# Optimization experiments

Measured on AMD Instinct MI355X. Metric: run time of the kernel, lower is better.

The kernel has to match this reference:

```python
import jax, jax.numpy as jnp
import numpy as np

DIM = 1024
EXP = 4
B, S = 4, 4096


def setup_inputs() -> dict:
    key = jax.random.key(0)
    ks = jax.random.split(key, 20)
    d, h = DIM, DIM * EXP
    sc = 1.0 / np.sqrt(d)
    inp = {
        "x": jax.random.normal(ks[0], (B, S, d), dtype=jnp.float32),
        # attention linears, stored [in, out] so y = x @ W + b
        "wq": jax.random.normal(ks[1], (d, d), jnp.float32) * sc,
        "bq": jnp.zeros((d,), jnp.float32),
        "wk": jax.random.normal(ks[2], (d, d), jnp.float32) * sc,
        "bk": jnp.zeros((d,), jnp.float32),
        "wv": jax.random.normal(ks[3], (d, d), jnp.float32) * sc,
        "bv": jnp.zeros((d,), jnp.float32),
        "wo": jax.random.normal(ks[4], (d, d), jnp.float32) * sc,
        "bo": jnp.zeros((d,), jnp.float32),
        # FFN
        "w1": jax.random.normal(ks[5], (d, h), jnp.float32) * sc,
        "b1": jnp.zeros((h,), jnp.float32),
        "w2": jax.random.normal(ks[6], (h, d), jnp.float32) * (1.0 / np.sqrt(h)),
        "b2": jnp.zeros((d,), jnp.float32),
        # LayerNorms
        "g1": jnp.ones((d,), jnp.float32),
        "beta1": jnp.zeros((d,), jnp.float32),
        "g2": jnp.ones((d,), jnp.float32),
        "beta2": jnp.zeros((d,), jnp.float32),
    }
    return inp


def _layernorm(x, g, b, eps=1e-5):
    mu = jnp.mean(x, axis=-1, keepdims=True)
    var = jnp.mean(jnp.square(x - mu), axis=-1, keepdims=True)
    return (x - mu) * jax.lax.rsqrt(var + eps) * g + b


def _block(x, wq, bq, wk, bk, wv, bv, wo, bo, w1, b1, w2, b2, g1, beta1, g2, beta2):
    d = x.shape[-1]
    # attention sub-block (single head, full [B,S,S] scores as in source)
    h = _layernorm(x, g1, beta1)
    q = h @ wq + bq
    k = h @ wk + bk
    v = h @ wv + bv
    scores = jnp.einsum("bsd,btd->bst", q, k) / jnp.sqrt(jnp.asarray(d, x.dtype))
    attn = jax.nn.softmax(scores, axis=-1)
    a = jnp.einsum("bst,btd->bsd", attn, v) @ wo + bo
    x = x + a
    # FFN sub-block (exact GELU, matching torch nn.GELU default)
    h2 = _layernorm(x, g2, beta2)
    f = jax.nn.gelu(h2 @ w1 + b1, approximate=False) @ w2 + b2
    return x + f


def reference(x, wq, bq, wk, bk, wv, bv, wo, bo, w1, b1, w2, b2, g1, beta1, g2, beta2):
    return _block(x, wq, bq, wk, bk, wv, bv, wo, bo, w1, b1, w2, b2, g1, beta1, g2, beta2)
```

## Files before the change

kernel.cpp:

```cpp
#include <hip/hip_runtime.h>
#include <hip/hip_bf16.h>
#include <cstdint>

typedef __bf16 bf16;
typedef __bf16 bf16x8 __attribute__((ext_vector_type(8)));
typedef __bf16 bf16x4 __attribute__((ext_vector_type(4)));
typedef float f32x4 __attribute__((ext_vector_type(4)));

#define DEV __device__ __forceinline__

DEV float wred_sum(float v) {
#pragma unroll
  for (int off = 32; off > 0; off >>= 1) v += __shfl_xor(v, off, 64);
  return v;
}
DEV float wred_max(float v) {
#pragma unroll
  for (int off = 32; off > 0; off >>= 1) v = fmaxf(v, __shfl_xor(v, off, 64));
  return v;
}

__global__ void convT_kernel(const float* __restrict__ in, bf16* __restrict__ out,
                             int K, int N) {
  __shared__ float t[32][33];
  const int n0 = blockIdx.x * 32, k0 = blockIdx.y * 32;
  const int tx = threadIdx.x & 31, ty = threadIdx.x >> 5;
#pragma unroll
  for (int i = 0; i < 4; i++)
    t[ty + 8 * i][tx] = in[(long)(k0 + ty + 8 * i) * N + n0 + tx];
  __syncthreads();
#pragma unroll
  for (int i = 0; i < 4; i++)
    out[(long)(n0 + ty + 8 * i) * K + k0 + tx] = (bf16)t[tx][ty + 8 * i];
}

__global__ void transpose_bf16(const bf16* __restrict__ in, bf16* __restrict__ out,
                               int ldin, int ldout) {
  __shared__ bf16 t[32][33];
  const int c0 = blockIdx.x * 32, r0 = blockIdx.y * 32;
  const int tx = threadIdx.x & 31, ty = threadIdx.x >> 5;
#pragma unroll
  for (int i = 0; i < 4; i++)
    t[ty + 8 * i][tx] = in[(long)(r0 + ty + 8 * i) * ldin + c0 + tx];
  __syncthreads();
#pragma unroll
  for (int i = 0; i < 4; i++)
    out[(long)(c0 + ty + 8 * i) * ldout + r0 + tx] = t[tx][ty + 8 * i];
}

__global__ void ln_bf16_kernel(const float* __restrict__ x, const float* __restrict__ g,
                               const float* __restrict__ be, bf16* __restrict__ out) {
  const long row = blockIdx.x;
  const int tid = threadIdx.x;
  const float4 v = ((const float4*)(x + row * 1024))[tid];
  float s = v.x + v.y + v.z + v.w;
  float s2 = v.x * v.x + v.y * v.y + v.z * v.z + v.w * v.w;
  __shared__ float rs_[4], rs2_[4];
  s = wred_sum(s);
  s2 = wred_sum(s2);
  const int wave = tid >> 6, lane = tid & 63;
  if (lane == 0) { rs_[wave] = s; rs2_[wave] = s2; }
  __syncthreads();
  s = rs_[0] + rs_[1] + rs_[2] + rs_[3];
  s2 = rs2_[0] + rs2_[1] + rs2_[2] + rs2_[3];
  const float mu = s * (1.0f / 1024.0f);
  const float var = s2 * (1.0f / 1024.0f) - mu * mu;
  const float rstd = rsqrtf(var + 1e-5f);
  const float4 gg = ((const float4*)g)[tid];
  const float4 bb = ((const float4*)be)[tid];
  bf16x4 o;
  o[0] = (bf16)((v.x - mu) * rstd * gg.x + bb.x);
  o[1] = (bf16)((v.y - mu) * rstd * gg.y + bb.y);
  o[2] = (bf16)((v.z - mu) * rstd * gg.z + bb.z);
  o[3] = (bf16)((v.w - mu) * rstd * gg.w + bb.w);
  *(bf16x4*)(out + row * 1024 + tid * 4) = o;
}

__global__ void softmax_kernel(bf16* __restrict__ p) {
  const long row = blockIdx.x;
  bf16* pr = p + row * 4096;
  const int tid = threadIdx.x;
  bf16x8 a = *(const bf16x8*)(pr + tid * 16);
  bf16x8 b = *(const bf16x8*)(pr + tid * 16 + 8);
  float v[16];
#pragma unroll
  for (int i = 0; i < 8; i++) { v[i] = (float)a[i]; v[8 + i] = (float)b[i]; }
  float mx = -1e30f;
#pragma unroll
  for (int i = 0; i < 16; i++) mx = fmaxf(mx, v[i]);
  __shared__ float red1[4], red2[4];
  mx = wred_max(mx);
  const int wave = tid >> 6, lane = tid & 63;
  if (lane == 0) red1[wave] = mx;
  __syncthreads();
  mx = fmaxf(fmaxf(red1[0], red1[1]), fmaxf(red1[2], red1[3]));
  float s = 0.0f;
#pragma unroll
  for (int i = 0; i < 16; i++) { v[i] = __expf(v[i] - mx); s += v[i]; }
  s = wred_sum(s);
  if (lane == 0) red2[wave] = s;
  __syncthreads();
  s = red2[0] + red2[1] + red2[2] + red2[3];
  const float inv = 1.0f / s;
#pragma unroll
  for (int i = 0; i < 8; i++) { a[i] = (bf16)(v[i] * inv); b[i] = (bf16)(v[8 + i] * inv); }
  *(bf16x8*)(pr + tid * 16) = a;
  *(bf16x8*)(pr + tid * 16 + 8) = b;
}

enum { EPI_BF16 = 0, EPI_QKV = 1, EPI_GELU = 2, EPI_F32RES = 3 };

DEV void stage16(const bf16* g, bf16* l) {
  __builtin_amdgcn_global_load_lds((const __attribute__((address_space(1))) void*)g,
                                   (__attribute__((address_space(3))) void*)l, 16, 0, 0);
}

template <int EPI>
__global__ __launch_bounds__(256)
void gemm128(const bf16* __restrict__ A, const bf16* __restrict__ B,
             const float* __restrict__ bias, const float* __restrict__ resid,
             void* Cout, int M, int N, int K,
             int lda, int ldb, int ldc, float alpha) {
  extern __shared__ __align__(16) char smem[];
  bf16* sA = (bf16*)smem;
  bf16* sB = sA + 3 * 8192;
  int flat = (int)(blockIdx.y * gridDim.x + blockIdx.x);
  {
    const int nwg = (int)(gridDim.x * gridDim.y);
    const int qq = nwg >> 3, rr = nwg & 7;
    const int xcd = flat & 7, idx = flat >> 3;
    flat = (xcd < rr ? xcd * (qq + 1) : rr * (qq + 1) + (xcd - rr) * qq) + idx;
  }
  const int bix = flat % (int)gridDim.x, biy = flat / (int)gridDim.x;
  const int tid = threadIdx.x;
  const int lane = tid & 63;
  const int wid = tid >> 6;
  const int q = lane >> 4, r16 = lane & 15;
  const int wr = wid >> 1, wc = wid & 1;
  const long m0 = (long)biy * 128;
  const long n0 = (long)bix * 128;
  const int srow = tid >> 3;
  const int gcol = ((tid & 7) ^ (srow & 7)) * 8;
  const long lda32 = (long)lda * 32, ldb32 = (long)ldb * 32;
  const bf16* Ag = A + (m0 + srow) * (long)lda + gcol;
  const bf16* Bg = B + (n0 + srow) * (long)ldb + gcol;
  const int NT = K >> 6;
  const int swz = r16 * 64 + ((q ^ (r16 & 7)) * 8);
  const int abase = wr * 4096 + swz;
  const int bbase = wc * 4096 + swz;
  f32x4 acc[4][4] = {};

#pragma unroll
  for (int blk = 0; blk < 4; ++blk) {
    stage16(Ag + blk * lda32, sA + tid * 8 + blk * 2048);
    stage16(Bg + blk * ldb32, sB + tid * 8 + blk * 2048);
  }
  if (NT > 1) {
#pragma unroll
    for (int blk = 0; blk < 4; ++blk) {
      stage16(Ag + 64 + blk * lda32, sA + 8192 + tid * 8 + blk * 2048);
      stage16(Bg + 64 + blk * ldb32, sB + 8192 + tid * 8 + blk * 2048);
    }
    asm volatile("s_waitcnt vmcnt(8)" ::: "memory");
  } else {
    asm volatile("s_waitcnt vmcnt(0)" ::: "memory");
  }
  __builtin_amdgcn_sched_barrier(0);
  __builtin_amdgcn_s_barrier();
  __builtin_amdgcn_sched_barrier(0);

  int bx = 0, bs = 16384;
  for (int t = 0; t < NT; ++t) {
    if (t + 2 < NT) {
      const bf16* Agn = Ag + (t + 2) * 64;
      const bf16* Bgn = Bg + (t + 2) * 64;
#pragma unroll
      for (int blk = 0; blk < 4; ++blk) {
        stage16(Agn + blk * lda32, sA + bs + tid * 8 + blk * 2048);
        stage16(Bgn + blk * ldb32, sB + bs + tid * 8 + blk * 2048);
      }
    }
    const bf16* sAb = sA + bx;
    const bf16* sBb = sB + bx;
    bf16x8 a0[4], a1[4], b0[4], b1[4];
#pragma unroll
    for (int i = 0; i < 4; ++i) {
      a0[i] = *(const bf16x8*)(sAb + (abase + i * 1024));
      a1[i] = *(const bf16x8*)(sAb + ((abase + i * 1024) ^ 32));
      b0[i] = *(const bf16x8*)(sBb + (bbase + i * 1024));
      b1[i] = *(const bf16x8*)(sBb + ((bbase + i * 1024) ^ 32));
    }
#pragma unroll
    for (int i = 0; i < 4; ++i)
#pragma unroll
      for (int j = 0; j < 4; ++j) {
        acc[i][j] = __builtin_amdgcn_mfma_f32_16x16x32_bf16(b0[j], a0[i], acc[i][j], 0, 0, 0);
        acc[i][j] = __builtin_amdgcn_mfma_f32_16x16x32_bf16(b1[j], a1[i], acc[i][j], 0, 0, 0);
      }
    if (t + 2 < NT) {
      asm volatile("s_waitcnt vmcnt(8)" ::: "memory");
    } else if (t + 1 < NT) {
      asm volatile("s_waitcnt vmcnt(0)" ::: "memory");
    }
    if (t + 1 < NT) {
      __builtin_amdgcn_sched_barrier(0);
      __builtin_amdgcn_s_barrier();
      __builtin_amdgcn_sched_barrier(0);
    }
    bx += 8192; if (bx == 24576) bx = 0;
    bs += 8192; if (bs == 24576) bs = 0;
  }

#pragma unroll
  for (int i = 0; i < 4; ++i) {
    const long row = m0 + wr * 64 + i * 16 + r16;
#pragma unroll
    for (int j = 0; j < 4; ++j) {
      const int ncol = (int)n0 + wc * 64 + j * 16 + q * 4;
      float4 b4 = make_float4(0.f, 0.f, 0.f, 0.f);
      if (bias != nullptr) b4 = *(const float4*)(bias + ncol);
      float v0 = acc[i][j][0] * alpha + b4.x;
      float v1 = acc[i][j][1] * alpha + b4.y;
      float v2 = acc[i][j][2] * alpha + b4.z;
      float v3 = acc[i][j][3] * alpha + b4.w;
      if (EPI == EPI_F32RES) {
        const long idx = row * (long)ldc + ncol;
        const float4 rr = *(const float4*)(resid + idx);
        const float4 o = make_float4(v0 + rr.x, v1 + rr.y, v2 + rr.z, v3 + rr.w);
        *(float4*)((float*)Cout + idx) = o;
      } else {
        bf16x4 o;
        o[0] = (bf16)v0; o[1] = (bf16)v1; o[2] = (bf16)v2; o[3] = (bf16)v3;
        *(bf16x4*)((bf16*)Cout + row * (long)ldc + ncol) = o;
      }
    }
  }
}

template <int EPI>
__global__ __launch_bounds__(512, 2)
void gemm256(const bf16* __restrict__ A, const bf16* __restrict__ B,
             const float* __restrict__ bias, const float* bias2, const float* bias3,
             const float* resid, void* Cout, int M, int N, int K,
             int lda, int ldb, int ldc, float alpha) {
  extern __shared__ __align__(16) char smem[];
  bf16* sA = (bf16*)smem;
  bf16* sB = sA + 32768;
  const int tid = threadIdx.x;
  const int lane = tid & 63;
  const int wid = tid >> 6;
  const int q = lane >> 4, r16 = lane & 15;
  const int wr = wid >> 2, wc = wid & 3;
  const long m0 = (long)blockIdx.y * 256;
  const long n0 = (long)blockIdx.x * 256;
  const int srow = tid >> 3;
  const int gcol = ((tid & 7) ^ (srow & 7)) * 8;
  const long lda64 = (long)lda * 64, ldb64 = (long)ldb * 64;
  const bf16* AgT = A + (m0 + srow) * (long)lda + gcol;
  const bf16* BgT = B + (n0 + srow) * (long)ldb + gcol;
  bf16* lA = sA + tid * 8;
  bf16* lB = sB + tid * 8;
  const int NT = K >> 6;
  const int swz = r16 * 64 + ((q ^ (r16 & 7)) * 8);
  const int abase = wr * 8192 + swz;
  const int bbase = (wc >> 1) * 8192 + (wc & 1) * 4096 + swz;

  f32x4 acc[8][4] = {};

  stage16(BgT,             lB);
  stage16(BgT + ldb64,     lB + 4096);
  stage16(BgT + 2 * ldb64, lB + 8192);
  stage16(BgT + 3 * ldb64, lB + 12288);
  stage16(AgT,             lA);
  stage16(AgT + lda64,     lA + 4096);
  stage16(AgT + 2 * lda64, lA + 8192);
  stage16(AgT + 3 * lda64, lA + 12288);
  if (NT > 1) {
    stage16(BgT + 64,             lB + 16384);
    stage16(BgT + 64 + ldb64,     lB + 16384 + 4096);
    stage16(BgT + 64 + 2 * ldb64, lB + 16384 + 8192);
    stage16(BgT + 64 + 3 * ldb64, lB + 16384 + 12288);
    asm volatile("s_waitcnt vmcnt(4)" ::: "memory");
  } else {
    asm volatile("s_waitcnt vmcnt(0)" ::: "memory");
  }
  __builtin_amdgcn_sched_barrier(0);
  __builtin_amdgcn_s_barrier();
  __builtin_amdgcn_sched_barrier(0);

  for (int t = 0; t < NT; ++t) {
    const int bx = (t & 1) * 16384;
    const int nbx = 16384 - bx;
    const bf16* sAb = sA + bx;
    const bf16* sBb = sB + bx;
    bf16x8 b0[4], b1[4];
#pragma unroll
    for (int p = 0; p < 4; ++p) {
      if (p == 0) {
#pragma unroll
        for (int n = 0; n < 4; ++n) {
          b0[n] = *(const bf16x8*)(sBb + (bbase + n * 1024));
          b1[n] = *(const bf16x8*)(sBb + ((bbase + n * 1024) ^ 32));
        }
      }
      const int ab = abase + p * 2048;
      const bf16x8 a00 = *(const bf16x8*)(sAb + ab);
      const bf16x8 a10 = *(const bf16x8*)(sAb + (ab ^ 32));
      const bf16x8 a01 = *(const bf16x8*)(sAb + (ab + 1024));
      const bf16x8 a11 = *(const bf16x8*)(sAb + ((ab + 1024) ^ 32));
      if (p == 0 && t + 1 < NT) {
        stage16(AgT + 64,         lA + nbx);
        stage16(AgT + 64 + lda64, lA + nbx + 4096);
      }
      if (p == 1 && t + 1 < NT) {
        stage16(AgT + 64 + 2 * lda64, lA + nbx + 8192);
        stage16(AgT + 64 + 3 * lda64, lA + nbx + 12288);
      }
      if (p == 2 && t + 2 < NT) {
        stage16(BgT + 128,         lB + bx);
        stage16(BgT + 128 + ldb64, lB + bx + 4096);
      }
      if (p == 3 && t + 2 < NT) {
        stage16(BgT + 128 + 2 * ldb64, lB + bx + 8192);
        stage16(BgT + 128 + 3 * ldb64, lB + bx + 12288);
      }
      __builtin_amdgcn_sched_barrier(0);
      __builtin_amdgcn_s_barrier();
      __builtin_amdgcn_sched_barrier(0);
      __builtin_amdgcn_s_setprio(1);
#pragma unroll
      for (int n = 0; n < 4; ++n) {
        acc[2 * p][n]     = __builtin_amdgcn_mfma_f32_16x16x32_bf16(b0[n], a00, acc[2 * p][n], 0, 0, 0);
        acc[2 * p][n]     = __builtin_amdgcn_mfma_f32_16x16x32_bf16(b1[n], a10, acc[2 * p][n], 0, 0, 0);
        acc[2 * p + 1][n] = __builtin_amdgcn_mfma_f32_16x16x32_bf16(b0[n], a01, acc[2 * p + 1][n], 0, 0, 0);
        acc[2 * p + 1][n] = __builtin_amdgcn_mfma_f32_16x16x32_bf16(b1[n], a11, acc[2 * p + 1][n], 0, 0, 0);
      }
      __builtin_amdgcn_s_setprio(0);
      if (p == 3) {
        if (t + 2 < NT)      asm volatile("s_waitcnt vmcnt(4)" ::: "memory");
        else if (t + 1 < NT) asm volatile("s_waitcnt vmcnt(0)" ::: "memory");
      }
      __builtin_amdgcn_sched_barrier(0);
      __builtin_amdgcn_s_barrier();
      __builtin_amdgcn_sched_barrier(0);
    }
    AgT += 64;
    BgT += 64;
  }

#pragma unroll
  for (int m = 0; m < 8; ++m) {
    const long row = m0 + wr * 128 + m * 16 + r16;
#pragma unroll
    for (int n = 0; n < 4; ++n) {
      const int ncol = (int)n0 + wc * 64 + n * 16 + q * 4;
      float4 b4 = make_float4(0.f, 0.f, 0.f, 0.f);
      if (EPI == EPI_QKV) {
        const int band = ncol >> 10;
        const float* bsel = band == 0 ? bias : (band == 1 ? bias2 : bias3);
        b4 = *(const float4*)(bsel + (ncol & 1023));
      } else if (bias != nullptr) {
        b4 = *(const float4*)(bias + ncol);
      }
      float v0 = acc[m][n][0] * alpha + b4.x;
      float v1 = acc[m][n][1] * alpha + b4.y;
      float v2 = acc[m][n][2] * alpha + b4.z;
      float v3 = acc[m][n][3] * alpha + b4.w;
      if (EPI == EPI_GELU) {
        v0 = 0.5f * v0 * (1.0f + erff(v0 * 0.70710678118654752f));
        v1 = 0.5f * v1 * (1.0f + erff(v1 * 0.70710678118654752f));
        v2 = 0.5f * v2 * (1.0f + erff(v2 * 0.70710678118654752f));
        v3 = 0.5f * v3 * (1.0f + erff(v3 * 0.70710678118654752f));
      }
      if (EPI == EPI_F32RES) {
        const long idx = row * (long)ldc + ncol;
        const float4 rr = *(const float4*)(resid + idx);
        const float4 o = make_float4(v0 + rr.x, v1 + rr.y, v2 + rr.z, v3 + rr.w);
        *(float4*)((float*)Cout + idx) = o;
      } else {
        bf16x4 o;
        o[0] = (bf16)v0; o[1] = (bf16)v1; o[2] = (bf16)v2; o[3] = (bf16)v3;
        *(bf16x4*)((bf16*)Cout + row * (long)ldc + ncol) = o;
      }
    }
  }
}

extern "C" void kernel_launch(void* const* d_in, const int* in_sizes, int n_in,
                              void* d_out, int out_size, void* d_ws, size_t ws_size,
                              hipStream_t stream) {
  const float* x  = (const float*)d_in[0];
  const float* wq = (const float*)d_in[1];
  const float* bq = (const float*)d_in[2];
  const float* wk = (const float*)d_in[3];
  const float* bk = (const float*)d_in[4];
  const float* wv = (const float*)d_in[5];
  const float* bv = (const float*)d_in[6];
  const float* wo = (const float*)d_in[7];
  const float* bo = (const float*)d_in[8];
  const float* w1 = (const float*)d_in[9];
  const float* b1 = (const float*)d_in[10];
  const float* w2 = (const float*)d_in[11];
  const float* b2 = (const float*)d_in[12];
  const float* g1 = (const float*)d_in[13];
  const float* be1 = (const float*)d_in[14];
  const float* g2 = (const float*)d_in[15];
  const float* be2 = (const float*)d_in[16];

  static int attr_done = 0;
  if (!attr_done) {
    attr_done = 1;
    hipFuncSetAttribute(reinterpret_cast<const void*>(&gemm256<EPI_QKV>),
                        hipFuncAttributeMaxDynamicSharedMemorySize, 131072);
    hipFuncSetAttribute(reinterpret_cast<const void*>(&gemm256<EPI_BF16>),
                        hipFuncAttributeMaxDynamicSharedMemorySize, 131072);
    hipFuncSetAttribute(reinterpret_cast<const void*>(&gemm256<EPI_GELU>),
                        hipFuncAttributeMaxDynamicSharedMemorySize, 131072);
    hipFuncSetAttribute(reinterpret_cast<const void*>(&gemm256<EPI_F32RES>),
                        hipFuncAttributeMaxDynamicSharedMemorySize, 131072);
    hipFuncSetAttribute(reinterpret_cast<const void*>(&gemm128<EPI_BF16>),
                        hipFuncAttributeMaxDynamicSharedMemorySize, 98304);
    hipFuncSetAttribute(reinterpret_cast<const void*>(&gemm128<EPI_F32RES>),
                        hipFuncAttributeMaxDynamicSharedMemorySize, 98304);
  }

  const long MB = 1 << 20;
  char* ws = (char*)d_ws;
  char* ob = (char*)d_out;
  bf16* WQKV = (bf16*)(ws + 0 * MB);
  bf16* WO   = (bf16*)(ws + 6 * MB);
  bf16* W1   = (bf16*)(ws + 8 * MB);
  bf16* W2   = (bf16*)(ws + 16 * MB);
  bf16* H    = (bf16*)(ws + 24 * MB);
  bf16* P    = (bf16*)(ob + 0 * MB);
  bf16* QKVb = (bf16*)(ob + 32 * MB);
  bf16* Vt   = (bf16*)(ob + 56 * MB);
  float* OUT = (float*)d_out;
  const dim3 blk(256);
  const dim3 blk512(512);
  const size_t SMEM = 131072;
  const size_t SMEM128 = 98304;

  convT_kernel<<<dim3(32, 32), blk, 0, stream>>>(wq, WQKV, 1024, 1024);
  convT_kernel<<<dim3(32, 32), blk, 0, stream>>>(wk, WQKV + 1024 * 1024, 1024, 1024);
  convT_kernel<<<dim3(32, 32), blk, 0, stream>>>(wv, WQKV + 2048 * 1024, 1024, 1024);
  convT_kernel<<<dim3(32, 32), blk, 0, stream>>>(wo, WO, 1024, 1024);
  convT_kernel<<<dim3(128, 32), blk, 0, stream>>>(w1, W1, 1024, 4096);
  convT_kernel<<<dim3(32, 128), blk, 0, stream>>>(w2, W2, 4096, 1024);
  ln_bf16_kernel<<<16384, blk, 0, stream>>>(x, g1, be1, H);
  for (int z = 0; z < 4; z++) {
    const long zo = (long)z * 4096 * 1024;
    gemm256<EPI_QKV><<<dim3(12, 16), blk512, SMEM, stream>>>(
        H + zo, WQKV, bq, bk, bv, nullptr, QKVb,
        4096, 3072, 1024, 1024, 1024, 3072, 1.0f);
    transpose_bf16<<<dim3(32, 128), blk, 0, stream>>>(QKVb + 2048, Vt, 3072, 4096);
    gemm256<EPI_BF16><<<dim3(16, 16), blk512, SMEM, stream>>>(
        QKVb, QKVb + 1024, nullptr, nullptr, nullptr, nullptr, P,
        4096, 4096, 1024, 3072, 3072, 4096, 1.0f / 32.0f);
    softmax_kernel<<<4096, blk, 0, stream>>>(P);
    gemm128<EPI_BF16><<<dim3(8, 32), blk, SMEM128, stream>>>(
        P, Vt, nullptr, nullptr, H + zo,
        4096, 1024, 4096, 4096, 4096, 1024, 1.0f);
  }
  gemm256<EPI_F32RES><<<dim3(4, 64), blk512, SMEM, stream>>>(
      H, WO, bo, nullptr, nullptr, x, OUT,
      16384, 1024, 1024, 1024, 1024, 1024, 1.0f);
  bf16* H2m = (bf16*)(ws + 0 * MB);
  bf16* Fm  = (bf16*)(ws + 24 * MB);
  for (int mc = 0; mc < 4; mc++) {
    const long ro = (long)mc * 4096 * 1024;
    ln_bf16_kernel<<<4096, blk, 0, stream>>>(OUT + ro, g2, be2, H2m);
    gemm256<EPI_GELU><<<dim3(16, 16), blk512, SMEM, stream>>>(
        H2m, W1, b1, nullptr, nullptr, nullptr, Fm,
        4096, 4096, 1024, 1024, 1024, 4096, 1.0f);
    gemm128<EPI_F32RES><<<dim3(8, 32), blk, SMEM128, stream>>>(
        Fm, W2, b2, OUT + ro, OUT + ro,
        4096, 1024, 4096, 4096, 4096, 1024, 1.0f);
  }
  (void)in_sizes; (void)n_in; (void)out_size; (void)ws_size;
}
```

Measured before the change: 1.248 ms.

## Deepen gemm128 prefetch to four LDS stages and reorder gemm256 staging

gemm128 moves from a 3-stage to a 4-stage LDS ring, prefetching three K-tiles ahead, and grows its LDS allocation to 128KB. gemm256 reorders its global-to-LDS loads so the second A tile is staged up front and later A/B loads are interleaved differently across the four sub-phases, with a new partial vmcnt wait mid-iteration. The aim is to hide more global load latency behind MFMA work. The extra LDS in gemm128 may lower occupancy, and the hand-counted vmcnt values must match the new issue order exactly.

```diff
diff --git a/kernel.cpp b/kernel.cpp
--- a/kernel.cpp
+++ b/kernel.cpp
@@ -123,7 +123,7 @@
              int lda, int ldb, int ldc, float alpha) {
   extern __shared__ __align__(16) char smem[];
   bf16* sA = (bf16*)smem;
-  bf16* sB = sA + 3 * 8192;
+  bf16* sB = sA + 4 * 8192;
   int flat = (int)(blockIdx.y * gridDim.x + blockIdx.x);
   {
     const int nwg = (int)(gridDim.x * gridDim.y);
@@ -150,30 +150,27 @@
   const int bbase = wc * 4096 + swz;
   f32x4 acc[4][4] = {};
 
-#pragma unroll
-  for (int blk = 0; blk < 4; ++blk) {
-    stage16(Ag + blk * lda32, sA + tid * 8 + blk * 2048);
-    stage16(Bg + blk * ldb32, sB + tid * 8 + blk * 2048);
-  }
-  if (NT > 1) {
+  const int PRE = NT < 3 ? NT : 3;
+  for (int tt = 0; tt < PRE; ++tt) {
 #pragma unroll
     for (int blk = 0; blk < 4; ++blk) {
-      stage16(Ag + 64 + blk * lda32, sA + 8192 + tid * 8 + blk * 2048);
-      stage16(Bg + 64 + blk * ldb32, sB + 8192 + tid * 8 + blk * 2048);
-    }
-    asm volatile("s_waitcnt vmcnt(8)" ::: "memory");
-  } else {
-    asm volatile("s_waitcnt vmcnt(0)" ::: "memory");
-  }
+      stage16(Ag + tt * 64 + blk * lda32, sA + tt * 8192 + tid * 8 + blk * 2048);
+      stage16(Bg + tt * 64 + blk * ldb32, sB + tt * 8192 + tid * 8 + blk * 2048);
+    }
+  }
+  if (NT >= 3)      asm volatile("s_waitcnt vmcnt(16)" ::: "memory");
+  else if (NT == 2) asm volatile("s_waitcnt vmcnt(8)" ::: "memory");
+  else              asm volatile("s_waitcnt vmcnt(0)" ::: "memory");
   __builtin_amdgcn_sched_barrier(0);
   __builtin_amdgcn_s_barrier();
   __builtin_amdgcn_sched_barrier(0);
 
-  int bx = 0, bs = 16384;
   for (int t = 0; t < NT; ++t) {
-    if (t + 2 < NT) {
-      const bf16* Agn = Ag + (t + 2) * 64;
-      const bf16* Bgn = Bg + (t + 2) * 64;
+    const int bx = (t & 3) * 8192;
+    if (t + 3 < NT) {
+      const int bs = ((t + 3) & 3) * 8192;
+      const bf16* Agn = Ag + (t + 3) * 64;
+      const bf16* Bgn = Bg + (t + 3) * 64;
 #pragma unroll
       for (int blk = 0; blk < 4; ++blk) {
         stage16(Agn + blk * lda32, sA + bs + tid * 8 + blk * 2048);
@@ -197,18 +194,14 @@
         acc[i][j] = __builtin_amdgcn_mfma_f32_16x16x32_bf16(b0[j], a0[i], acc[i][j], 0, 0, 0);
         acc[i][j] = __builtin_amdgcn_mfma_f32_16x16x32_bf16(b1[j], a1[i], acc[i][j], 0, 0, 0);
       }
-    if (t + 2 < NT) {
-      asm volatile("s_waitcnt vmcnt(8)" ::: "memory");
-    } else if (t + 1 < NT) {
-      asm volatile("s_waitcnt vmcnt(0)" ::: "memory");
-    }
+    if (t + 3 < NT)      asm volatile("s_waitcnt vmcnt(16)" ::: "memory");
+    else if (t + 2 < NT) asm volatile("s_waitcnt vmcnt(8)" ::: "memory");
+    else if (t + 1 < NT) asm volatile("s_waitcnt vmcnt(0)" ::: "memory");
     if (t + 1 < NT) {
       __builtin_amdgcn_sched_barrier(0);
       __builtin_amdgcn_s_barrier();
       __builtin_amdgcn_sched_barrier(0);
     }
-    bx += 8192; if (bx == 24576) bx = 0;
-    bs += 8192; if (bs == 24576) bs = 0;
   }
 
 #pragma unroll
@@ -267,20 +260,24 @@
 
   f32x4 acc[8][4] = {};
 
-  stage16(BgT,             lB);
-  stage16(BgT + ldb64,     lB + 4096);
-  stage16(BgT + 2 * ldb64, lB + 8192);
-  stage16(BgT + 3 * ldb64, lB + 12288);
-  stage16(AgT,             lA);
-  stage16(AgT + lda64,     lA + 4096);
-  stage16(AgT + 2 * lda64, lA + 8192);
-  stage16(AgT + 3 * lda64, lA + 12288);
+  stage16(AgT,              lA);
+  stage16(AgT + 2 * lda64,  lA + 8192);
+  stage16(AgT + lda64,      lA + 4096);
+  stage16(AgT + 3 * lda64,  lA + 12288);
+  stage16(BgT,              lB);
+  stage16(BgT + ldb64,      lB + 4096);
+  stage16(BgT + 2 * ldb64,  lB + 8192);
+  stage16(BgT + 3 * ldb64,  lB + 12288);
   if (NT > 1) {
+    stage16(AgT + 64,             lA + 16384);
+    stage16(AgT + 64 + 2 * lda64, lA + 16384 + 8192);
     stage16(BgT + 64,             lB + 16384);
     stage16(BgT + 64 + ldb64,     lB + 16384 + 4096);
     stage16(BgT + 64 + 2 * ldb64, lB + 16384 + 8192);
     stage16(BgT + 64 + 3 * ldb64, lB + 16384 + 12288);
-    asm volatile("s_waitcnt vmcnt(4)" ::: "memory");
+    stage16(AgT + 64 + lda64,     lA + 16384 + 4096);
+    stage16(AgT + 64 + 3 * lda64, lA + 16384 + 12288);
+    asm volatile("s_waitcnt vmcnt(8)" ::: "memory");
   } else {
     asm volatile("s_waitcnt vmcnt(0)" ::: "memory");
   }
@@ -293,6 +290,8 @@
     const int nbx = 16384 - bx;
     const bf16* sAb = sA + bx;
     const bf16* sBb = sB + bx;
+    const long k1 = (long)(t + 1) * 64;
+    const long k2 = (long)(t + 2) * 64;
     bf16x8 b0[4], b1[4];
 #pragma unroll
     for (int p = 0; p < 4; ++p) {
@@ -308,21 +307,21 @@
       const bf16x8 a10 = *(const bf16x8*)(sAb + (ab ^ 32));
       const bf16x8 a01 = *(const bf16x8*)(sAb + (ab + 1024));
       const bf16x8 a11 = *(const bf16x8*)(sAb + ((ab + 1024) ^ 32));
-      if (p == 0 && t + 1 < NT) {
-        stage16(AgT + 64,         lA + nbx);
-        stage16(AgT + 64 + lda64, lA + nbx + 4096);
-      }
-      if (p == 1 && t + 1 < NT) {
-        stage16(AgT + 64 + 2 * lda64, lA + nbx + 8192);
-        stage16(AgT + 64 + 3 * lda64, lA + nbx + 12288);
+      if (p == 0 && t >= 1 && t + 1 < NT) {
+        stage16(AgT + k1 + lda64,     lA + nbx + 4096);
+        stage16(AgT + k1 + 3 * lda64, lA + nbx + 12288);
+      }
+      if (p == 1 && t + 2 < NT) {
+        stage16(BgT + k2,         lB + bx);
+        stage16(BgT + k2 + ldb64, lB + bx + 4096);
       }
       if (p == 2 && t + 2 < NT) {
-        stage16(BgT + 128,         lB + bx);
-        stage16(BgT + 128 + ldb64, lB + bx + 4096);
+        stage16(AgT + k2,             lA + bx);
+        stage16(AgT + k2 + 2 * lda64, lA + bx + 8192);
       }
       if (p == 3 && t + 2 < NT) {
-        stage16(BgT + 128 + 2 * ldb64, lB + bx + 8192);
-        stage16(BgT + 128 + 3 * ldb64, lB + bx + 12288);
+        stage16(BgT + k2 + 2 * ldb64, lB + bx + 8192);
+        stage16(BgT + k2 + 3 * ldb64, lB + bx + 12288);
       }
       __builtin_amdgcn_sched_barrier(0);
       __builtin_amdgcn_s_barrier();
@@ -336,16 +335,19 @@
         acc[2 * p + 1][n] = __builtin_amdgcn_mfma_f32_16x16x32_bf16(b1[n], a11, acc[2 * p + 1][n], 0, 0, 0);
       }
       __builtin_amdgcn_s_setprio(0);
+      if (p == 1) {
+        if (t + 2 < NT)      asm volatile("s_waitcnt vmcnt(10)" ::: "memory");
+        else if (t + 1 < NT) asm volatile("s_waitcnt vmcnt(8)" ::: "memory");
+        else                 asm volatile("s_waitcnt vmcnt(0)" ::: "memory");
+      }
       if (p == 3) {
-        if (t + 2 < NT)      asm volatile("s_waitcnt vmcnt(4)" ::: "memory");
-        else if (t + 1 < NT) asm volatile("s_waitcnt vmcnt(0)" ::: "memory");
+        if (t + 2 < NT)      asm volatile("s_waitcnt vmcnt(8)" ::: "memory");
+        else if (t + 1 < NT) asm volatile("s_waitcnt vmcnt(2)" ::: "memory");
       }
       __builtin_amdgcn_sched_barrier(0);
       __builtin_amdgcn_s_barrier();
       __builtin_amdgcn_sched_barrier(0);
     }
-    AgT += 64;
-    BgT += 64;
   }
 
 #pragma unroll
@@ -419,9 +421,9 @@
     hipFuncSetAttribute(reinterpret_cast<const void*>(&gemm256<EPI_F32RES>),
                         hipFuncAttributeMaxDynamicSharedMemorySize, 131072);
     hipFuncSetAttribute(reinterpret_cast<const void*>(&gemm128<EPI_BF16>),
-                        hipFuncAttributeMaxDynamicSharedMemorySize, 98304);
+                        hipFuncAttributeMaxDynamicSharedMemorySize, 131072);
     hipFuncSetAttribute(reinterpret_cast<const void*>(&gemm128<EPI_F32RES>),
-                        hipFuncAttributeMaxDynamicSharedMemorySize, 98304);
+                        hipFuncAttributeMaxDynamicSharedMemorySize, 131072);
   }
 
   const long MB = 1 << 20;
@@ -439,7 +441,7 @@
   const dim3 blk(256);
   const dim3 blk512(512);
   const size_t SMEM = 131072;
-  const size_t SMEM128 = 98304;
+  const size_t SMEM128 = 131072;
 
   convT_kernel<<<dim3(32, 32), blk, 0, stream>>>(wq, WQKV, 1024, 1024);
   convT_kernel<<<dim3(32, 32), blk, 0, stream>>>(wk, WQKV + 1024 * 1024, 1024, 1024);
```

Result: no change. 1.257 ms (+0.7%).
